# Kernel tuning notes

Hardware: AMD Instinct MI355X
Metric: run time of the kernel (lower is better)

The kernel has to match this reference:

```python
import jax, jax.numpy as jnp
import numpy as np
import math

N = 1500; E = 24000; C_IN = 16; H = 64; NUM_LAYERS = 10; RATIO = 0.9
NEG = -1e9


def setup_inputs() -> dict:
    key = jax.random.key(0)
    ks = jax.random.split(key, 40)
    it = iter(range(40))
    def nrm(shape, scale=0.1):
        return jax.random.normal(ks[next(it)], shape, dtype=jnp.float32) * scale
    src = jax.random.randint(ks[next(it)], (E,), 0, N, dtype=jnp.int32)
    off = jax.random.randint(ks[next(it)], (E,), 1, N, dtype=jnp.int32)
    dst = (src + off) % N  # no self loops in the raw edge list
    return dict(
        x=nrm((N, C_IN), 1.0),
        edge_src=src, edge_dst=dst,
        W1=nrm((C_IN, H // 2)), b1=jnp.zeros((H // 2,), jnp.float32),
        W2=nrm((H // 2, H)), b2=jnp.zeros((H,), jnp.float32),
        W3=nrm((H, H)), b3=jnp.zeros((H,), jnp.float32),
        Wrel=nrm((NUM_LAYERS - 1, H, H)), brel=jnp.zeros((NUM_LAYERS - 1, H), jnp.float32),
        Wroot=nrm((NUM_LAYERS - 1, H, H)),
        pW=nrm((4, H, H)), pb=jnp.zeros((4, H), jnp.float32),
        leW1=nrm((4, H, 1)), leb1=jnp.zeros((4, 1), jnp.float32),
        leW2=nrm((4, H, 1)),
        leW3=nrm((4, H, 1)), leb3=jnp.zeros((4, 1), jnp.float32),
        linW1=nrm((NUM_LAYERS * H, H)), linb1=jnp.zeros((H,), jnp.float32),
        linW2=nrm((H, 10)), linb2=jnp.zeros((10,), jnp.float32),
    )


def _seg_mean(vals, idx, n):
    s = jax.ops.segment_sum(vals, idx, num_segments=n)
    c = jax.ops.segment_sum(jnp.ones((idx.shape[0],), vals.dtype), idx, num_segments=n)
    return s / jnp.maximum(c, 1.0)[:, None]


def _feast(x, W, b, srcL, dstL, n):
    # FeaStConv with heads=1: softmax over a single head == 1 -> mean of lin(x_j) + bias
    return _seg_mean((x @ W)[srcL], dstL, n) + b


def _gconv_sparse(x, src, dst, Wr, br, Wo, n):
    return _seg_mean(x[src], dst, n) @ Wr + br + x @ Wo


def _gconv_dense(x, A, Wr, br, Wo):
    # mean aggregation: divide weighted sum by count of (nonzero) in-edges
    Mf = (A != 0).astype(x.dtype)
    agg = (A.T @ x) / jnp.maximum(Mf.sum(0), 1.0)[:, None]
    return agg @ Wr + br + x @ Wo


def _topk_pool(xc, fitness, ratio):
    k = int(math.ceil(ratio * xc.shape[0]))
    fit_k, perm = jax.lax.top_k(fitness, k)
    return xc[perm] * fit_k[:, None], perm


def _asap_sparse(x, src, dst, pW, pb, leW1, leb1, leW2, leW3, leb3):
    n = x.shape[0]
    ar = jnp.arange(n, dtype=src.dtype)
    srcL = jnp.concatenate([src, ar])  # add remaining self loops (weight 1)
    dstL = jnp.concatenate([dst, ar])
    xq = jax.ops.segment_max(x[srcL], dstL, num_segments=n) @ pW + pb
    s = jax.nn.leaky_relu(jnp.sum(xq[dstL] * x[srcL], -1), 0.2)
    m = jax.ops.segment_max(s, dstL, num_segments=n)
    e = jnp.exp(s - m[dstL])
    score = e / jax.ops.segment_sum(e, dstL, num_segments=n)[dstL]
    xc = jax.ops.segment_sum(x[srcL] * score[:, None], dstL, num_segments=n)
    # LEConv fitness score (edge weight = 1)
    a = xc @ leW1 + leb1
    b = xc @ leW2
    agg = jax.ops.segment_sum(a[srcL] - b[dstL], dstL, num_segments=n)
    fitness = jax.nn.sigmoid((agg + xc @ leW3 + leb3)[:, 0])
    x_new, perm = _topk_pool(xc, fitness, RATIO)
    S = jnp.zeros((n, n), x.dtype).at[srcL, dstL].add(score)
    A = jnp.zeros((n, n), x.dtype).at[srcL, dstL].add(1.0)
    Sp = S[:, perm]
    A_new = Sp.T @ A @ Sp
    k = A_new.shape[0]
    return x_new, A_new * (1.0 - jnp.eye(k, dtype=x.dtype))  # remove diag


def _asap_dense(x, A, pW, pb, leW1, leb1, leW2, leW3, leb3):
    n = x.shape[0]
    A = A + jnp.diag((jnp.diag(A) == 0).astype(A.dtype))  # add remaining self loops
    M = A != 0
    Mf = M.astype(x.dtype)
    xq = jnp.max(jnp.where(M[:, :, None], x[:, None, :], NEG), axis=0) @ pW + pb  # [n,H]
    Sc = jnp.where(M, jax.nn.leaky_relu(x @ xq.T, 0.2), NEG)  # [j,i]
    m = Sc.max(0)
    e = jnp.where(M, jnp.exp(Sc - m), 0.0)
    score = e / e.sum(0)
    xc = score.T @ x
    a = xc @ leW1 + leb1
    b = xc @ leW2
    agg = Mf.T @ a - Mf.sum(0)[:, None] * b
    fitness = jax.nn.sigmoid((agg + xc @ leW3 + leb3)[:, 0])
    x_new, perm = _topk_pool(xc, fitness, RATIO)
    Sp = score[:, perm]
    A_new = Sp.T @ A @ Sp
    k = A_new.shape[0]
    return x_new, A_new * (1.0 - jnp.eye(k, dtype=x.dtype))


def _forward(x, edge_src, edge_dst, W1, b1, W2, b2, W3, b3, Wrel, brel, Wroot,
             pW, pb, leW1, leb1, leW2, leW3, leb3, linW1, linb1, linW2, linb2):
    n = x.shape[0]
    ar = jnp.arange(n, dtype=edge_src.dtype)
    srcL = jnp.concatenate([edge_src, ar])  # FeaStConv add_self_loops=True
    dstL = jnp.concatenate([edge_dst, ar])
    x = jax.nn.elu(_feast(x, W1, b1, srcL, dstL, n))
    x = jax.nn.elu(_feast(x, W2, b2, srcL, dstL, n))
    x = jax.nn.elu(_feast(x, W3, b3, srcL, dstL, n))
    xs = [x.mean(0, keepdims=True)]  # single graph -> global_mean_pool == mean
    A = None
    for i in range(NUM_LAYERS - 1):
        if A is None:
            x = jax.nn.relu(_gconv_sparse(x, edge_src, edge_dst, Wrel[i], brel[i], Wroot[i], x.shape[0]))
        else:
            x = jax.nn.relu(_gconv_dense(x, A, Wrel[i], brel[i], Wroot[i]))
        xs.append(x.mean(0, keepdims=True))
        if i % 2 == 0 and i < NUM_LAYERS - 2:
            p = i // 2
            args = (pW[p], pb[p], leW1[p], leb1[p], leW2[p], leW3[p], leb3[p])
            if A is None:
                x, A = _asap_sparse(x, edge_src, edge_dst, *args)
            else:
                x, A = _asap_dense(x, A, *args)
    h = jnp.concatenate(xs, axis=-1)  # [1, NUM_LAYERS*H] jumping-knowledge cat
    h = jax.nn.relu(h @ linW1 + linb1)
    return jax.nn.log_softmax(h @ linW2 + linb2, axis=-1)


def reference(x, edge_src, edge_dst, W1, b1, W2, b2, W3, b3, Wrel, brel, Wroot,
              pW, pb, leW1, leb1, leW2, leW3, leb3, linW1, linb1, linW2, linb2):
    return _forward(x, edge_src, edge_dst, W1, b1, W2, b2, W3, b3, Wrel, brel, Wroot,
                    pW, pb, leW1, leb1, leW2, leW3, leb3, linW1, linb1, linW2, linb2)
```

## Files before the change

### kernel.cpp

```cpp
#include <hip/hip_runtime.h>
#include <math.h>

#define NEGV -1000000000.0f

typedef short short8 __attribute__((ext_vector_type(8)));
typedef float floatx4 __attribute__((ext_vector_type(4)));

__device__ __forceinline__ float sigm(float x){ return 1.0f/(1.0f+expf(-x)); }
__device__ __forceinline__ void edge_sd(int e,const int* src,const int* dst,int E,int& s,int& d){
  if(e<E){ s=src[e]; d=dst[e]; } else { s=e-E; d=s; }
}
__device__ __forceinline__ ushort bf16rn(float x){
  unsigned u = __float_as_uint(x);
  unsigned r = (u + 0x7fffu + ((u>>16)&1u)) >> 16;
  return (ushort)r;
}
__device__ __forceinline__ float bf16f(ushort h){ return __uint_as_float(((unsigned)h)<<16); }

__global__ void k_zero(float* __restrict__ p, size_t n){
  size_t i = (size_t)blockIdx.x*256 + threadIdx.x;
  if (i < n) p[i] = 0.0f;
}

__global__ void k_split3(const float* __restrict__ src,int R,int Cs,int ld,
                         ushort* __restrict__ dst,int Cp,int bmode){
  int idx = blockIdx.x*256+threadIdx.x;
  if (idx >= R*Cp) return;
  int r = idx / Cp, c = idx - r*Cp;
  float x = (c < Cs) ? src[(size_t)r*ld + c] : 0.0f;
  ushort h = bf16rn(x);
  ushort l = bf16rn(x - bf16f(h));
  size_t base = (size_t)r*(3*Cp) + c;
  dst[base]        = h;
  dst[base + Cp]   = bmode ? l : h;
  dst[base + 2*Cp] = bmode ? h : l;
}
__global__ void k_split3_Tdual(const float* __restrict__ src,int Rs,int Cs,int ld,
                               const int* __restrict__ gperm,const float* __restrict__ cscale,
                               const float* __restrict__ emax,
                               ushort* __restrict__ dstA,ushort* __restrict__ dstB,
                               ushort* __restrict__ dstCpad,int Kp){
  __shared__ float t[32][33];
  int tx = threadIdx.x & 31, ty = threadIdx.x >> 5;
  int kb = blockIdx.y*32, xb = blockIdx.x*32;
  int x = xb + tx;
  int gx = (x < Cs) ? gperm[x] : 0;
#pragma unroll
  for (int i=0;i<4;i++){
    int k = kb + ty + i*8;
    t[ty+i*8][tx] = (k < Rs && x < Cs) ? src[(size_t)k*ld + gx] : 0.0f;
  }
  __syncthreads();
  const int K3 = 3*Kp;
#pragma unroll
  for (int i=0;i<4;i++){
    int xo = xb + ty + i*8, ko = kb + tx;
    if (xo < Cs){
      float v = 0.0f;
      if (ko < Rs){
        int g = gperm[xo];
        v = expf(t[tx][ty+i*8] - emax[g]) * cscale[g];
      }
      ushort h = bf16rn(v);
      ushort l = bf16rn(v - bf16f(h));
      size_t base = (size_t)xo*K3 + ko;
      dstA[base] = h; dstA[base+Kp] = h; dstA[base+2*Kp] = l;
      dstB[base] = h; dstB[base+Kp] = l; dstB[base+2*Kp] = h;
      if (ko >= Rs){ dstCpad[base]=0; dstCpad[base+Kp]=0; dstCpad[base+2*Kp]=0; }
    }
  }
}

template<int EPI>
__global__ __launch_bounds__(256) void k_gemm_mfma(
    const ushort* __restrict__ A, const ushort* __restrict__ B,
    float* __restrict__ C, int ldc, int M, int N, int K3,
    const float* __restrict__ mask, int ldm)
{
  __shared__ ushort As[2][64][72];
  __shared__ ushort Bs[2][64][72];
  const int tid = threadIdx.x;
  const int m0 = blockIdx.y*64, n0 = blockIdx.x*64;
  const int w = tid>>6, lane = tid&63;
  const int lo4 = lane&15, quad = lane>>4;
  const int sr = tid>>2, sseg = tid&3;

  floatx4 acc[4];
#pragma unroll
  for(int c=0;c<4;c++){ acc[c][0]=0.f; acc[c][1]=0.f; acc[c][2]=0.f; acc[c][3]=0.f; }

  const size_t arow = (size_t)(m0+sr)*K3;
  const size_t brow = (size_t)(n0+sr)*K3;
  const bool aval = (m0+sr) < M;
  const bool bval = (n0+sr) < N;

  uint4 av0 = make_uint4(0,0,0,0), av1 = make_uint4(0,0,0,0);
  uint4 bv0 = make_uint4(0,0,0,0), bv1 = make_uint4(0,0,0,0);
  if (aval){ av0 = *(const uint4*)(A + arow + sseg*8);
             av1 = *(const uint4*)(A + arow + 32 + sseg*8); }
  if (bval){ bv0 = *(const uint4*)(B + brow + sseg*8);
             bv1 = *(const uint4*)(B + brow + 32 + sseg*8); }
  *(uint4*)&As[0][sr][sseg*8] = av0; *(uint4*)&As[0][sr][32+sseg*8] = av1;
  *(uint4*)&Bs[0][sr][sseg*8] = bv0; *(uint4*)&Bs[0][sr][32+sseg*8] = bv1;
  __syncthreads();

  const int T = K3 >> 6;
  for (int i=0;i<T;i++){
    const int cb = i & 1;
    if (i+1 < T){
      const int k0 = (i+1)<<6;
      av0 = make_uint4(0,0,0,0); av1 = make_uint4(0,0,0,0);
      bv0 = make_uint4(0,0,0,0); bv1 = make_uint4(0,0,0,0);
      if (aval){ av0 = *(const uint4*)(A + arow + k0 + sseg*8);
                 av1 = *(const uint4*)(A + arow + k0 + 32 + sseg*8); }
      if (bval){ bv0 = *(const uint4*)(B + brow + k0 + sseg*8);
                 bv1 = *(const uint4*)(B + brow + k0 + 32 + sseg*8); }
    }
    short8 af0 = *(const short8*)&As[cb][16*w + lo4][quad*8];
    short8 af1 = *(const short8*)&As[cb][16*w + lo4][32+quad*8];
#pragma unroll
    for (int c=0;c<4;c++){
      short8 bf0 = *(const short8*)&Bs[cb][16*c + lo4][quad*8];
      acc[c] = __builtin_amdgcn_mfma_f32_16x16x32_bf16(af0, bf0, acc[c], 0, 0, 0);
      short8 bf1 = *(const short8*)&Bs[cb][16*c + lo4][32+quad*8];
      acc[c] = __builtin_amdgcn_mfma_f32_16x16x32_bf16(af1, bf1, acc[c], 0, 0, 0);
    }
    if (i+1 < T){
      __syncthreads();
      *(uint4*)&As[1-cb][sr][sseg*8] = av0; *(uint4*)&As[1-cb][sr][32+sseg*8] = av1;
      *(uint4*)&Bs[1-cb][sr][sseg*8] = bv0; *(uint4*)&Bs[1-cb][sr][32+sseg*8] = bv1;
      __syncthreads();
    }
  }

#pragma unroll
  for (int c=0;c<4;c++){
    const int gn = n0 + 16*c + lo4;
#pragma unroll
    for (int r=0;r<4;r++){
      const int gm = m0 + 16*w + quad*4 + r;
      if (gm < M && gn < N){
        float v = acc[c][r];
        if (EPI==1) v = (mask[(size_t)gm*ldm+gn] != 0.0f || gm==gn) ? (v > 0.0f ? v : 0.2f*v) : NEGV;
        if (EPI==2 && gm==gn) v = 0.0f;
        C[(size_t)gm*ldc+gn] = v;
      }
    }
  }
}

__global__ __launch_bounds__(256) void k_gemm_mfma_tb(
    const ushort* __restrict__ A, const ushort* __restrict__ B,
    ushort* __restrict__ Cb, int Kp, int M, int N, int K3)
{
  __shared__ ushort As[2][64][72];
  __shared__ ushort Bs[2][64][72];
  const int tid = threadIdx.x;
  const int m0 = blockIdx.y*64, n0 = blockIdx.x*64;
  const int w = tid>>6, lane = tid&63;
  const int lo4 = lane&15, quad = lane>>4;
  const int sr = tid>>2, sseg = tid&3;

  floatx4 acc[4];
#pragma unroll
  for(int c=0;c<4;c++){ acc[c][0]=0.f; acc[c][1]=0.f; acc[c][2]=0.f; acc[c][3]=0.f; }

  const size_t arow = (size_t)(m0+sr)*K3;
  const size_t brow = (size_t)(n0+sr)*K3;
  const bool aval = (m0+sr) < M;
  const bool bval = (n0+sr) < N;

  uint4 av0 = make_uint4(0,0,0,0), av1 = make_uint4(0,0,0,0);
  uint4 bv0 = make_uint4(0,0,0,0), bv1 = make_uint4(0,0,0,0);
  if (aval){ av0 = *(const uint4*)(A + arow + sseg*8);
             av1 = *(const uint4*)(A + arow + 32 + sseg*8); }
  if (bval){ bv0 = *(const uint4*)(B + brow + sseg*8);
             bv1 = *(const uint4*)(B + brow + 32 + sseg*8); }
  *(uint4*)&As[0][sr][sseg*8] = av0; *(uint4*)&As[0][sr][32+sseg*8] = av1;
  *(uint4*)&Bs[0][sr][sseg*8] = bv0; *(uint4*)&Bs[0][sr][32+sseg*8] = bv1;
  __syncthreads();

  const int T = K3 >> 6;
  for (int i=0;i<T;i++){
    const int cb = i & 1;
    if (i+1 < T){
      const int k0 = (i+1)<<6;
      av0 = make_uint4(0,0,0,0); av1 = make_uint4(0,0,0,0);
      bv0 = make_uint4(0,0,0,0); bv1 = make_uint4(0,0,0,0);
      if (aval){ av0 = *(const uint4*)(A + arow + k0 + sseg*8);
                 av1 = *(const uint4*)(A + arow + k0 + 32 + sseg*8); }
      if (bval){ bv0 = *(const uint4*)(B + brow + k0 + sseg*8);
                 bv1 = *(const uint4*)(B + brow + k0 + 32 + sseg*8); }
    }
    short8 af0 = *(const short8*)&As[cb][16*w + lo4][quad*8];
    short8 af1 = *(const short8*)&As[cb][16*w + lo4][32+quad*8];
#pragma unroll
    for (int c=0;c<4;c++){
      short8 bf0 = *(const short8*)&Bs[cb][16*c + lo4][quad*8];
      acc[c] = __builtin_amdgcn_mfma_f32_16x16x32_bf16(af0, bf0, acc[c], 0, 0, 0);
      short8 bf1 = *(const short8*)&Bs[cb][16*c + lo4][32+quad*8];
      acc[c] = __builtin_amdgcn_mfma_f32_16x16x32_bf16(af1, bf1, acc[c], 0, 0, 0);
    }
    if (i+1 < T){
      __syncthreads();
      *(uint4*)&As[1-cb][sr][sseg*8] = av0; *(uint4*)&As[1-cb][sr][32+sseg*8] = av1;
      *(uint4*)&Bs[1-cb][sr][sseg*8] = bv0; *(uint4*)&Bs[1-cb][sr][32+sseg*8] = bv1;
      __syncthreads();
    }
  }

  const int K3o = 3*Kp;
#pragma unroll
  for (int c=0;c<4;c++){
    const int gn = n0 + 16*c + lo4;
    if (gn < N){
#pragma unroll
      for (int r=0;r<4;r++){
        const int gm = m0 + 16*w + quad*4 + r;
        if (gm < M){
          size_t base = (size_t)gn*K3o + gm;
          float sp = bf16f(B[base]) + bf16f(B[base+Kp]);
          float v = acc[c][r] + sp;
          ushort h = bf16rn(v);
          ushort l = bf16rn(v - bf16f(h));
          Cb[base] = h; Cb[base+Kp] = l; Cb[base+2*Kp] = h;
        }
      }
    }
  }
}

template<bool MAXM, bool COUNT, bool EXPM, bool SELF>
__global__ __launch_bounds__(256) void k_skinny(
    const float* __restrict__ A, int lda,
    const float* __restrict__ X,
    const float* __restrict__ mcol,
    float* __restrict__ P, int* __restrict__ cntp,
    int M, int K, int kchunk)
{
  __shared__ float As[16][68];
  __shared__ float Xs[16][68];
  const int tid = threadIdx.x;
  const int m0 = blockIdx.y * 64;
  const int tmb = (tid & 15) * 4, tnb = (tid >> 4) * 4;
  float acc[4][4];
  int cacc[4] = {0,0,0,0};
#pragma unroll
  for (int i=0;i<4;i++)
#pragma unroll
    for (int j=0;j<4;j++) acc[i][j] = MAXM ? NEGV : 0.0f;

  const int kstart = blockIdx.z * kchunk;
  int kend = kstart + kchunk; if (kend > K) kend = K;
  const int ml = tid & 63, tb = tid >> 6;
  const bool mvalid = (m0 + ml) < M;
  float mc = 0.0f;
  if (EXPM && mvalid) mc = mcol[m0 + ml];

  for (int k0 = kstart; k0 < kend; k0 += 16) {
#pragma unroll
    for (int s=0;s<4;s++) {
      const int tk = tb + s*4;
      float va = 0.0f, vx = 0.0f;
      if ((k0+tk) < K) {
        if (mvalid){
          va = A[(size_t)(k0+tk)*lda + m0 + ml];
          if (EXPM) va = expf(va - mc);
        }
        vx = X[(size_t)(k0+tk)*64 + ml];
      }
      As[tk][ml] = va;
      Xs[tk][ml] = vx;
    }
    __syncthreads();
#pragma unroll
    for (int kk=0; kk<16; kk++) {
      const float4 a4 = *(const float4*)&As[kk][tmb];
      const float4 b4 = *(const float4*)&Xs[kk][tnb];
      const float av[4] = {a4.x,a4.y,a4.z,a4.w};
      const float bv[4] = {b4.x,b4.y,b4.z,b4.w};
#pragma unroll
      for (int i=0;i<4;i++){
        if (COUNT) cacc[i] += (av[i] != 0.0f) ? 1 : 0;
#pragma unroll
        for (int j=0;j<4;j++) {
          if (MAXM) acc[i][j] = fmaxf(acc[i][j], av[i] != 0.0f ? bv[j] : NEGV);
          else      acc[i][j] = fmaf(av[i], bv[j], acc[i][j]);
        }
      }
    }
    __syncthreads();
  }

  const size_t slab = (size_t)blockIdx.z * M * 64;
#pragma unroll
  for (int i=0;i<4;i++){
    const int m = m0 + tmb + i;
    if (m < M){
#pragma unroll
      for (int j=0;j<4;j++){
        float v = acc[i][j];
        if (SELF) v = fmaxf(v, X[(size_t)m*64 + tnb + j]);
        P[slab + (size_t)m*64 + tnb + j] = v;
      }
    }
  }
  if (COUNT && tnb == 0){
#pragma unroll
    for (int i=0;i<4;i++){
      const int m = m0 + tmb + i;
      if (m < M) cntp[blockIdx.z*M + m] = cacc[i];
    }
  }
}

__global__ __launch_bounds__(256) void k_poolq(
    const float* __restrict__ SEGP,const int* __restrict__ cntp8,int Z,
    const float* __restrict__ pWp,const float* __restrict__ pbp,
    const float* __restrict__ X,
    ushort* __restrict__ dstA,ushort* __restrict__ dstB,
    float* __restrict__ cntP,int n)
{
  __shared__ float xq[4][65];
  const int tid = threadIdx.x;
  const int r = tid>>6, j = tid&63;
  const int i = blockIdx.x*4 + r;
  float v = NEGV;
  if (i < n){
    for(int z=0;z<Z;z++) v = fmaxf(v, SEGP[(size_t)z*n*64 + (size_t)i*64 + j]);
    if (j == 0){
      int c=1; for(int z=0;z<Z;z++) c += cntp8[z*n+i];
      cntP[i] = (float)c;
    }
  }
  xq[r][j] = v;
  __syncthreads();
  if (i < n){
    float s = pbp[j];
    for(int q=0;q<64;q++) s = fmaf(xq[r][q], pWp[q*64+j], s);
    size_t base = (size_t)i*192 + j;
    ushort h = bf16rn(s), l = bf16rn(s - bf16f(h));
    dstB[base] = h; dstB[base+64] = l; dstB[base+128] = h;
    float x = X[(size_t)i*64 + j];
    h = bf16rn(x); l = bf16rn(x - bf16f(h));
    dstA[base] = h; dstA[base+64] = h; dstA[base+128] = l;
  }
}

__global__ __launch_bounds__(256) void k_gconv_fuse(
    const float* __restrict__ SEGP,const int* __restrict__ cntp8,int Z,
    const float* __restrict__ Wrel,const float* __restrict__ brel,
    const float* __restrict__ X,const float* __restrict__ Wroot,
    float* __restrict__ XN,int n,float* __restrict__ meanacc,float inv_n)
{
  __shared__ float agg_s[4][65];
  __shared__ float xrow[4][65];
  __shared__ float cnt_s[4];
  const int tid = threadIdx.x;
  const int r = tid>>6, j = tid&63;
  const int i = blockIdx.x*4 + r;
  float a = 0.0f;
  if (i < n){
    for(int z=0;z<Z;z++) a += SEGP[(size_t)z*n*64 + (size_t)i*64 + j];
    xrow[r][j] = X[(size_t)i*64 + j];
    if (j == 0){
      int c=0; for(int z=0;z<Z;z++) c += cntp8[z*n+i];
      cnt_s[r] = (float)(c>1?c:1);
    }
  }
  agg_s[r][j] = a;
  __syncthreads();
  float v = 0.0f;
  if (i < n){
    float acc=0.0f, rt=0.0f;
    for(int q=0;q<64;q++){
      acc = fmaf(agg_s[r][q], Wrel[q*64+j], acc);
      rt  = fmaf(xrow[r][q],  Wroot[q*64+j], rt);
    }
    v = fmaxf(acc/cnt_s[r] + brel[j] + rt, 0.0f);
    XN[(size_t)i*64 + j] = v;
  }
  __syncthreads();
  agg_s[r][j] = v;
  __syncthreads();
  if (r == 0) atomicAdd(&meanacc[j], (agg_s[0][j]+agg_s[1][j]+agg_s[2][j]+agg_s[3][j])*inv_n);
}

__global__ __launch_bounds__(256) void k_smax_fused(const float* __restrict__ S,int n,
                                                    float* __restrict__ mcol,float* __restrict__ invd){
  __shared__ float red[16][17];
  const int jc = threadIdx.x & 15, rg = threadIdx.x >> 4;
  const int j = blockIdx.x*16 + jc;
  float m = -3.0e38f;
  if (j < n)
    for(int i=rg;i<n;i+=16) m = fmaxf(m, S[(size_t)i*n+j]);
  red[rg][jc] = m;
  __syncthreads();
  for(int s=8;s>0;s>>=1){
    if(rg<s) red[rg][jc] = fmaxf(red[rg][jc], red[rg+s][jc]);
    __syncthreads();
  }
  const float mc = red[0][jc];
  __syncthreads();
  float sum = 0.0f;
  if (j < n)
    for(int i=rg;i<n;i+=16) sum += expf(S[(size_t)i*n+j]-mc);
  red[rg][jc] = sum;
  __syncthreads();
  for(int s=8;s>0;s>>=1){
    if(rg<s) red[rg][jc] += red[rg+s][jc];
    __syncthreads();
  }
  if(rg==0 && j<n){ mcol[j]=mc; invd[j]=1.0f/red[0][jc]; }
}

__global__ __launch_bounds__(256) void k_xcabc_dense(
    const float* __restrict__ SEGP,int Z,const float* __restrict__ invd,
    float* __restrict__ XC,
    const float* __restrict__ w1,const float* bb1,const float* __restrict__ w2,
    const float* __restrict__ w3,const float* bb3,
    float* aN,float* bN,float* cN,int* pcnt,int n)
{
  __shared__ float xc[4][65];
  const int tid = threadIdx.x;
  const int r = tid>>6, j = tid&63;
  const int i = blockIdx.x*4 + r;
  if (blockIdx.x==0 && tid==0) *pcnt = 0;
  float v = 0.0f;
  if (i < n){
    for(int z=0;z<Z;z++) v += SEGP[(size_t)z*n*64 + (size_t)i*64 + j];
    v *= invd[i];
    XC[(size_t)i*64+j] = v;
  }
  xc[r][j] = v;
  __syncthreads();
  if (i < n && j < 3){
    float s = (j==0)?bb1[0]:((j==2)?bb3[0]:0.0f);
    const float* w = (j==0)?w1:((j==1)?w2:w3);
    for(int q=0;q<64;q++) s = fmaf(xc[r][q], w[q], s);
    if(j==0) aN[i]=s; else if(j==1) bN[i]=s; else cN[i]=s;
  }
}

__global__ void k_aggcol(const float* __restrict__ A,const float* __restrict__ aN,
                         float* __restrict__ aggp,int n){
  int idx = blockIdx.x*256+threadIdx.x; if(idx>=n*16) return;
  int j = idx % n, c = idx / n;
  int i0 = (int)(((long long)n*c)/16), i1 = (int)(((long long)n*(c+1))/16);
  float s = 0.0f;
  for(int i=i0;i<i1;i++) if(A[(size_t)i*n + j] != 0.0f) s += aN[i];
  aggp[c*n + j] = s;
}

template<int MODE>
__global__ __launch_bounds__(256) void k_rank_fused(
    const float* __restrict__ fit_in,
    const float* __restrict__ aggp,const float* __restrict__ cntP,
    const float* __restrict__ aN,const float* __restrict__ bN,const float* __restrict__ cN,
    const float* __restrict__ XC,float* __restrict__ XN,
    int n,int k,int* pcnt,int* perm)
{
  __shared__ float fs[1504];
  const int tid = threadIdx.x;
  for(int u=tid; u<n; u+=256){
    float f;
    if (MODE==0) f = fit_in[u];
    else {
      float a = aN[u];
      for(int c=0;c<16;c++) a += aggp[c*n+u];
      f = sigm(a - cntP[u]*bN[u] + cN[u]);
    }
    fs[u] = f;
  }
  __syncthreads();
  const int v = blockIdx.x*256+tid; if(v>=n) return;
  const float fv = fs[v]; int r = 0;
  for(int u=0;u<n;u++){ float fu = fs[u]; r += (fu > fv || (fu == fv && u < v)) ? 1 : 0; }
  if (r < k){
    int p = atomicAdd(pcnt,1);
    perm[p] = v;
    const float* src = XC + (size_t)v*64;
    float* d = XN + (size_t)p*64;
    for(int h=0;h<64;h++) d[h] = src[h]*fv;
  }
}

__global__ void k_deg(const int* __restrict__ src,const int* __restrict__ dst,int* indeg,int* outdeg,int E){
  int e = blockIdx.x*256+threadIdx.x; if(e>=E) return;
  atomicAdd(&indeg[dst[e]],1); atomicAdd(&outdeg[src[e]],1);
}
__global__ __launch_bounds__(256) void k_prefix2(const int* __restrict__ indeg,const int* __restrict__ outdeg,
                          int* offD,int* curD,int* offS,int* curS,int n){
  __shared__ int ds[1504];
  const int* dsrc = blockIdx.y ? outdeg : indeg;
  for(int u=threadIdx.x; u<n; u+=256) ds[u] = dsrc[u];
  __syncthreads();
  int t = blockIdx.x*256+threadIdx.x; if(t>n) return;
  int s = 0;
  for(int u=0;u<t;u++) s += ds[u]+1;
  if (blockIdx.y){ offS[t]=s; if(t<n) curS[t]=s; }
  else           { offD[t]=s; if(t<n) curD[t]=s; }
}
__global__ void k_csr_fill2(const int* src,const int* dst,
                            int* curS,int* colS,int* eidS,
                            int* curD,int* rowD,int* eidD,int E,int n){
  int e = blockIdx.x*256+threadIdx.x; if(e>=E+n) return;
  int s,d; edge_sd(e,src,dst,E,s,d);
  int p = atomicAdd(&curS[s],1); colS[p]=d; eidS[p]=e;
  int q = atomicAdd(&curD[d],1); rowD[q]=s; eidD[q]=e;
}

__global__ void k_mm_small(const float* __restrict__ A,const float* __restrict__ W,
                           const float* __restrict__ b,float* __restrict__ C,
                           int M,int K,int Np,int act){
  int idx = blockIdx.x*256+threadIdx.x; if(idx>=M*Np) return;
  int m = idx/Np, j = idx - m*Np;
  float s = b ? b[j] : 0.0f;
  const float* a = A + (size_t)m*K;
  for(int q=0;q<K;q++) s = fmaf(a[q], W[(size_t)q*Np + j], s);
  if(act==1) s = fmaxf(s, 0.0f);
  C[idx] = s;
}

__global__ void k_feast_gf(const float* __restrict__ Y,const int* __restrict__ offD,
                           const int* __restrict__ rowD,
                           const float* __restrict__ b,float* X,int n,int H,
                           float* __restrict__ meanacc,float inv_n){
  __shared__ float ms[4][64];
  int idx = blockIdx.x*256+threadIdx.x;
  float v = 0.0f;
  if(idx<n*H){
    int i = idx/H, h = idx - i*H;
    int p0 = offD[i], p1 = offD[i+1];
    float s = 0.0f;
    for(int p=p0;p<p1;p++) s += Y[(size_t)rowD[p]*H + h];
    float t = s/(float)(p1-p0) + b[h];
    v = t > 0.0f ? t : (expf(t)-1.0f);
    X[idx] = v;
  }
  if(meanacc){
    int r = threadIdx.x>>6, j = threadIdx.x&63;
    ms[r][j] = (idx<n*H) ? v : 0.0f;
    __syncthreads();
    if(r==0) atomicAdd(&meanacc[j], (ms[0][j]+ms[1][j]+ms[2][j]+ms[3][j])*inv_n);
  }
}

__global__ __launch_bounds__(256) void k_gconv_sparse_f(
    const float* __restrict__ X,const int* __restrict__ offD,const int* __restrict__ rowD,
    const int* __restrict__ eidD,int E,
    const float* __restrict__ Wrel,const float* __restrict__ brel,
    const float* __restrict__ Wroot,
    float* __restrict__ XN,int n,float* __restrict__ meanacc,float inv_n)
{
  __shared__ float agg_s[4][65];
  __shared__ float xrow[4][65];
  __shared__ float cnt_s[4];
  const int tid = threadIdx.x;
  const int r = tid>>6, j = tid&63;
  const int i = blockIdx.x*4 + r;
  float a = 0.0f;
  if (i < n){
    int p0 = offD[i], p1 = offD[i+1], c = 0;
    for(int p=p0;p<p1;p++){
      if (eidD[p] < E){ a += X[(size_t)rowD[p]*64 + j]; c++; }
    }
    xrow[r][j] = X[(size_t)i*64 + j];
    if (j == 0) cnt_s[r] = (float)(c>1?c:1);
  }
  agg_s[r][j] = a;
  __syncthreads();
  float v = 0.0f;
  if (i < n){
    float acc=0.0f, rt=0.0f;
    for(int q=0;q<64;q++){
      acc = fmaf(agg_s[r][q], Wrel[q*64+j], acc);
      rt  = fmaf(xrow[r][q],  Wroot[q*64+j], rt);
    }
    v = fmaxf(acc/cnt_s[r] + brel[j] + rt, 0.0f);
    XN[(size_t)i*64 + j] = v;
  }
  __syncthreads();
  agg_s[r][j] = v;
  __syncthreads();
  if (r == 0) atomicAdd(&meanacc[j], (agg_s[0][j]+agg_s[1][j]+agg_s[2][j]+agg_s[3][j])*inv_n);
}

__global__ __launch_bounds__(256) void k_xqmaxq(
    const float* __restrict__ X,const int* __restrict__ offD,const int* __restrict__ rowD,
    const float* __restrict__ pWp,const float* __restrict__ pbp,
    float* __restrict__ XQ2,int n)
{
  __shared__ float xq[4][65];
  const int tid = threadIdx.x;
  const int r = tid>>6, j = tid&63;
  const int i = blockIdx.x*4 + r;
  float v = -3.0e38f;
  if (i < n){
    int p0 = offD[i], p1 = offD[i+1];
    for(int p=p0;p<p1;p++) v = fmaxf(v, X[(size_t)rowD[p]*64 + j]);
  }
  xq[r][j] = v;
  __syncthreads();
  if (i < n){
    float s = pbp[j];
    for(int q=0;q<64;q++) s = fmaf(xq[r][q], pWp[q*64+j], s);
    XQ2[(size_t)i*64+j] = s;
  }
}

__global__ void k_edge_score(const int* __restrict__ src,const int* __restrict__ dst,
                             const float* __restrict__ XQ2,const float* __restrict__ X,
                             float* sE,int E,int n){
  int e = blockIdx.x*256+threadIdx.x; if(e>=E+n) return;
  int s,d; edge_sd(e,src,dst,E,s,d);
  const float* q = XQ2 + (size_t)d*64;
  const float* x = X + (size_t)s*64;
  float acc = 0.0f;
  for(int h=0;h<64;h++) acc = fmaf(q[h], x[h], acc);
  sE[e] = acc > 0.0f ? acc : 0.2f*acc;
}

__global__ void k_dstsoft(const int* __restrict__ offD,const int* __restrict__ eidD,
                          const float* __restrict__ sE,float* __restrict__ scE,int n){
  int i = blockIdx.x*256+threadIdx.x; if(i>=n) return;
  int p0 = offD[i], p1 = offD[i+1];
  float m = -3.0e38f;
  for(int p=p0;p<p1;p++) m = fmaxf(m, sE[eidD[p]]);
  float d = 0.0f;
  for(int p=p0;p<p1;p++) d += expf(sE[eidD[p]]-m);
  float inv = 1.0f/d;
  for(int p=p0;p<p1;p++){ int e = eidD[p]; scE[e] = expf(sE[e]-m)*inv; }
}

__global__ __launch_bounds__(256) void k_xcabc0(
    const int* __restrict__ offD,const int* __restrict__ rowD,const int* __restrict__ eidD,
    const float* __restrict__ scE,const float* __restrict__ X,
    float* __restrict__ XC,
    const float* __restrict__ w1,const float* bb1,const float* __restrict__ w2,
    const float* __restrict__ w3,const float* bb3,
    float* aN,float* bN,float* cN,int* pcnt,int n)
{
  __shared__ float xc[4][65];
  const int tid = threadIdx.x;
  const int r = tid>>6, j = tid&63;
  const int i = blockIdx.x*4 + r;
  if (blockIdx.x==0 && tid==0) *pcnt = 0;
  float v = 0.0f;
  if (i < n){
    int p0 = offD[i], p1 = offD[i+1];
    for(int p=p0;p<p1;p++) v += scE[eidD[p]] * X[(size_t)rowD[p]*64 + j];
    XC[(size_t)i*64+j] = v;
  }
  xc[r][j] = v;
  __syncthreads();
  if (i < n && j < 3){
    float s = (j==0)?bb1[0]:((j==2)?bb3[0]:0.0f);
    const float* w = (j==0)?w1:((j==1)?w2:w3);
    for(int q=0;q<64;q++) s = fmaf(xc[r][q], w[q], s);
    if(j==0) aN[i]=s; else if(j==1) bN[i]=s; else cN[i]=s;
  }
}

__global__ void k_aggfit0(const int* __restrict__ offD,const int* __restrict__ rowD,
                          const float* aN,const float* bN,const float* cN,
                          float* fit,int n){
  int i = blockIdx.x*256+threadIdx.x; if(i>=n) return;
  int p0 = offD[i], p1 = offD[i+1];
  float s = 0.0f;
  for(int p=p0;p<p1;p++) s += aN[rowD[p]];
  fit[i] = sigm(s - (float)(p1-p0)*bN[i] + cN[i]);
}

__global__ void k_stage1n(const int* src,const int* dst,const int* __restrict__ offS,
                          const int* __restrict__ colS,const int* __restrict__ eidS,
                          const float* __restrict__ scE,
                          float* R,int E,int n){
  int e = blockIdx.x*256+threadIdx.x; if(e>=E+n) return;
  int i,j; edge_sd(e,src,dst,E,i,j);
  int p0 = offS[j], p1 = offS[j+1];
  float* Ri = R + (size_t)i*n;
  for(int p=p0;p<p1;p++) atomicAdd(&Ri[colS[p]], scE[eidS[p]]);
}
__global__ void k_stage2p(const int* __restrict__ perm,const int* __restrict__ offD,
                          const int* __restrict__ rowD,const int* __restrict__ eidD,
                          const float* __restrict__ scE,
                          const float* __restrict__ R,float* A,int k,int n){
  int idx = blockIdx.x*256+threadIdx.x; if(idx>=k*k) return;
  int u = idx/k, v = idx - u*k;
  int d = perm[u], pv = perm[v];
  float acc = 0.0f;
  int p0 = offD[d], p1 = offD[d+1];
  for(int p=p0;p<p1;p++) acc = fmaf(scE[eidD[p]], R[(size_t)rowD[p]*n + pv], acc);
  A[idx] = (u==v) ? 0.0f : acc;
}

__global__ void k_head2(const float* __restrict__ xs,const float* __restrict__ W1,
                        const float* __restrict__ b1,const float* __restrict__ W2,
                        const float* __restrict__ b2,float* out){
  __shared__ float h2[64];
  __shared__ float lg[10];
  int t = threadIdx.x;
  float s = b1[t];
  for(int q=0;q<640;q++) s = fmaf(xs[q], W1[q*64+t], s);
  h2[t] = fmaxf(s, 0.0f);
  __syncthreads();
  if(t < 10){
    float s2 = b2[t];
    for(int k=0;k<64;k++) s2 = fmaf(h2[k], W2[k*10+t], s2);
    lg[t] = s2;
  }
  __syncthreads();
  if(t == 0){
    float mx = lg[0];
    for(int i=1;i<10;i++) mx = fmaxf(mx, lg[i]);
    float se = 0.0f;
    for(int i=0;i<10;i++) se += expf(lg[i]-mx);
    float lse = mx + logf(se);
    for(int i=0;i<10;i++) out[i] = lg[i]-lse;
  }
}

extern "C" void kernel_launch(void* const* d_in, const int* in_sizes, int n_in,
                              void* d_out, int out_size, void* d_ws, size_t ws_size,
                              hipStream_t stream) {
  const int N0 = 1500, E = 24000, Z = 16, L = E + N0;
  const float* x0   = (const float*)d_in[0];
  const int* esrc   = (const int*)d_in[1];
  const int* edst   = (const int*)d_in[2];
  const float* W1   = (const float*)d_in[3];  const float* b1   = (const float*)d_in[4];
  const float* W2   = (const float*)d_in[5];  const float* b2   = (const float*)d_in[6];
  const float* W3   = (const float*)d_in[7];  const float* b3   = (const float*)d_in[8];
  const float* Wrel = (const float*)d_in[9];  const float* brel = (const float*)d_in[10];
  const float* Wroot= (const float*)d_in[11];
  const float* pW   = (const float*)d_in[12]; const float* pb   = (const float*)d_in[13];
  const float* leW1 = (const float*)d_in[14]; const float* leb1 = (const float*)d_in[15];
  const float* leW2 = (const float*)d_in[16]; const float* leW3 = (const float*)d_in[17];
  const float* leb3 = (const float*)d_in[18];
  const float* linW1= (const float*)d_in[19]; const float* linb1= (const float*)d_in[20];
  const float* linW2= (const float*)d_in[21]; const float* linb2= (const float*)d_in[22];
  float* out = (float*)d_out;

  float* ws = (float*)d_ws;
  size_t cur = 0;
  auto allocF = [&](size_t nf)->float*{ float* p = ws + cur; cur += (nf + 15) & ~(size_t)15; return p; };
  float* xs   = allocF(640);
  int* indeg  = (int*)allocF(1504);
  int* outdeg = (int*)allocF(1504);
  float* Xa  = allocF(96000); float* Xb  = allocF(96000); float* Y   = allocF(96000);
  float* XQ2 = allocF(96000); float* XC  = allocF(96000);
  float* mcol = allocF(1504); float* invd = allocF(1504);
  float* aN = allocF(1504); float* bN = allocF(1504); float* cN = allocF(1504);
  float* fit = allocF(1504); float* cntP = allocF(1504);
  int* pcnt = (int*)allocF(16);
  int* perm = (int*)allocF(1504);
  int* offD = (int*)allocF(1504); int* offS = (int*)allocF(1504);
  int* curD = (int*)allocF(1504); int* curS = (int*)allocF(1504);
  int* colS = (int*)allocF(25504); int* eidS = (int*)allocF(25504);
  int* rowD = (int*)allocF(25504); int* eidD = (int*)allocF(25504);
  float* sE = allocF(25504); float* scE = allocF(25504);
  int* cntp8 = (int*)allocF((size_t)Z*1504);
  float* aggp = allocF(16*1504);
  float* SEGP = allocF((size_t)Z*1504*64);
  float* Rbig = allocF((size_t)1500*1500);
  float* SCb  = Rbig;
  float* A0  = allocF((size_t)1350*1350);
  float* A1s = allocF((size_t)1350*1350);
  const size_t BFSZ = (size_t)1350*4224/2 + 32;
  ushort* Abf = (ushort*)allocF(BFSZ);
  ushort* Bbf = (ushort*)allocF(BFSZ);
  ushort* Cbf = (ushort*)allocF(BFSZ);
  ushort* Dbf = (ushort*)allocF(BFSZ);

  dim3 B256(256);
  auto G1 = [&](size_t n){ return dim3((unsigned)((n + 255) / 256)); };
  auto ZF = [&](void* p, size_t nfloats){ k_zero<<<G1(nfloats),B256,0,stream>>>((float*)p, nfloats); };
  auto kcz = [&](int K){ return (int)(((K + Z*16 - 1) / (Z*16)) * 16); };

  ZF(xs, 640 + 1504 + 1504);
  k_deg<<<G1(E),B256,0,stream>>>(esrc, edst, indeg, outdeg, E);
  k_prefix2<<<dim3((N0+256)/256,2),B256,0,stream>>>(indeg, outdeg, offD, curD, offS, curS, N0);
  k_csr_fill2<<<G1(L),B256,0,stream>>>(esrc, edst, curS, colS, eidS, curD, rowD, eidD, E, N0);

  auto feast = [&](const float* xin,int cin,const float* W,const float* bb,int hh,float* xout,float* macc){
    k_mm_small<<<G1((size_t)N0*hh),B256,0,stream>>>(xin, W, nullptr, Y, N0, cin, hh, 0);
    k_feast_gf<<<G1((size_t)N0*hh),B256,0,stream>>>(Y, offD, rowD, bb, xout, N0, hh, macc, 1.0f/N0);
  };
  feast(x0, 16, W1, b1, 32, Xa, nullptr);
  feast(Xa, 32, W2, b2, 64, Xb, nullptr);
  feast(Xb, 64, W3, b3, 64, Xa, xs + 0);
  float* X = Xa; float* XN = Xb;

  k_gconv_sparse_f<<<dim3((N0+3)/4),B256,0,stream>>>(X, offD, rowD, eidD, E, Wrel, brel, Wroot,
                                                     XN, N0, xs + 64, 1.0f/N0);
  { float* t = X; X = XN; XN = t; }

  {
    const int n = 1500, kk = 1350;
    k_xqmaxq<<<dim3((n+3)/4),B256,0,stream>>>(X, offD, rowD, pW, pb, XQ2, n);
    k_edge_score<<<G1(L),B256,0,stream>>>(esrc, edst, XQ2, X, sE, E, n);
    k_dstsoft<<<G1(n),B256,0,stream>>>(offD, eidD, sE, scE, n);
    k_xcabc0<<<dim3((n+3)/4),B256,0,stream>>>(offD, rowD, eidD, scE, X, XC,
                                              leW1, leb1, leW2, leW3, leb3, aN, bN, cN, pcnt, n);
    k_aggfit0<<<G1(n),B256,0,stream>>>(offD, rowD, aN, bN, cN, fit, n);
    k_rank_fused<0><<<G1(n),B256,0,stream>>>(fit, nullptr, nullptr, nullptr, nullptr, nullptr,
                                             XC, XN, n, kk, pcnt, perm);
    ZF(Rbig, (size_t)n*n);
    k_stage1n<<<G1(L),B256,0,stream>>>(esrc, edst, offS, colS, eidS, scE, Rbig, E, n);
    k_stage2p<<<G1((size_t)kk*kk),B256,0,stream>>>(perm, offD, rowD, eidD, scE, Rbig, A0, kk, n);
    { float* t = X; X = XN; XN = t; }
  }

  float* Acur = A0; float* Aoth = A1s;
  int nn = 1350;

  auto gconv_dense = [&](int layer){
    dim3 g(1, (nn+63)/64, Z);
    k_skinny<false,true,false,false><<<g,B256,0,stream>>>(Acur, nn, X, nullptr, SEGP, cntp8, nn, nn, kcz(nn));
    k_gconv_fuse<<<dim3((nn+3)/4),B256,0,stream>>>(SEGP, cntp8, Z,
        Wrel + (size_t)layer*4096, brel + layer*64, X, Wroot + (size_t)layer*4096,
        XN, nn, xs + (size_t)(layer+1)*64, 1.0f/nn);
    { float* t = X; X = XN; XN = t; }
  };

  auto asap_dense = [&](int kk, int p){
    {
      dim3 g(1, (nn+63)/64, Z);
      k_skinny<true,true,false,true><<<g,B256,0,stream>>>(Acur, nn, X, nullptr, SEGP, cntp8, nn, nn, kcz(nn));
    }
    k_poolq<<<dim3((nn+3)/4),B256,0,stream>>>(SEGP, cntp8, Z, pW + (size_t)p*4096, pb + p*64,
                                              X, Abf, Bbf, cntP, nn);
    {
      dim3 g((nn+63)/64, (nn+63)/64);
      k_gemm_mfma<1><<<g,B256,0,stream>>>(Abf, Bbf, SCb, nn, nn, nn, 192, Acur, nn);
    }
    k_smax_fused<<<dim3((nn+15)/16),B256,0,stream>>>(SCb, nn, mcol, invd);
    {
      dim3 g(1, (nn+63)/64, Z);
      k_skinny<false,false,true,false><<<g,B256,0,stream>>>(SCb, nn, X, mcol, SEGP, nullptr, nn, nn, kcz(nn));
    }
    k_xcabc_dense<<<dim3((nn+3)/4),B256,0,stream>>>(SEGP, Z, invd, XC,
        leW1 + p*64, leb1 + p, leW2 + p*64, leW3 + p*64, leb3 + p, aN, bN, cN, pcnt, nn);
    k_aggcol<<<G1((size_t)nn*16),B256,0,stream>>>(Acur, aN, aggp, nn);
    k_rank_fused<1><<<G1(nn),B256,0,stream>>>(nullptr, aggp, cntP, aN, bN, cN,
                                              XC, XN, nn, kk, pcnt, perm);
    const int Kp = (nn + 63) & ~63;
    const int K3 = 3*Kp;
    k_split3<<<G1((size_t)nn*Kp),B256,0,stream>>>(Acur, nn, nn, nn, Abf, Kp, 0);
    { dim3 gt((kk+31)/32, Kp/32);
      k_split3_Tdual<<<gt,B256,0,stream>>>(SCb, nn, kk, nn, perm, invd, mcol, Dbf, Bbf, Cbf, Kp); }
    { dim3 g((kk+63)/64, (nn+63)/64);
      k_gemm_mfma_tb<<<g,B256,0,stream>>>(Abf, Bbf, Cbf, Kp, nn, kk, K3); }
    { dim3 g((kk+63)/64, (kk+63)/64);
      k_gemm_mfma<2><<<g,B256,0,stream>>>(Dbf, Cbf, Aoth, kk, kk, kk, K3, nullptr, 0); }
    { float* t = X; X = XN; XN = t; }
    { float* t = Acur; Acur = Aoth; Aoth = t; }
    nn = kk;
  };

  gconv_dense(1);
  gconv_dense(2);
  asap_dense(1215, 1);
  gconv_dense(3);
  gconv_dense(4);
  asap_dense(1094, 2);
  gconv_dense(5);
  gconv_dense(6);
  asap_dense(985, 3);
  gconv_dense(7);
  gconv_dense(8);

  k_head2<<<1,64,0,stream>>>(xs, linW1, linb1, linW2, linb2, out);
}
```

Measured before the change: 1.509 ms.

## Split-K the pooled adjacency GEMMs into two partials plus reduction kernels

The two MFMA GEMMs in dense ASAP pooling (A·S and Sᵀ·(AS)) now run as split-K over two z-slices that write fp32 partials. Separate reduction kernels sum the partials, apply the bf16 split epilogue (transposed through shared memory) and zero the diagonal. This roughly doubles the block count for these small ~1000² GEMMs to fill more CUs. It costs extra launches and partial-buffer traffic, and reuses scratch buffers (Rbig, Aoth, SEGP) for the partials. The shared-memory load row mapping is also permuted.

```diff
diff --git a/kernel.cpp b/kernel.cpp
--- a/kernel.cpp
+++ b/kernel.cpp
@@ -142,16 +142,16 @@
       if (gm < M && gn < N){
         float v = acc[c][r];
         if (EPI==1) v = (mask[(size_t)gm*ldm+gn] != 0.0f || gm==gn) ? (v > 0.0f ? v : 0.2f*v) : NEGV;
-        if (EPI==2 && gm==gn) v = 0.0f;
         C[(size_t)gm*ldc+gn] = v;
       }
     }
   }
 }
 
-__global__ __launch_bounds__(256) void k_gemm_mfma_tb(
+__global__ __launch_bounds__(256) void k_gemm_pp(
     const ushort* __restrict__ A, const ushort* __restrict__ B,
-    ushort* __restrict__ Cb, int Kp, int M, int N, int K3)
+    float* __restrict__ P0, float* __restrict__ P1, int ldp,
+    int M, int N, int K3, int kchunk)
 {
   __shared__ ushort As[2][64][72];
   __shared__ ushort Bs[2][64][72];
@@ -159,14 +159,23 @@
   const int m0 = blockIdx.y*64, n0 = blockIdx.x*64;
   const int w = tid>>6, lane = tid&63;
   const int lo4 = lane&15, quad = lane>>4;
-  const int sr = tid>>2, sseg = tid&3;
+  const int l6 = tid & 63;
+  const int rw = (((l6>>2)&3)<<1) | ((l6>>4)&1) | (((l6>>5)&1)<<3);
+  const int sr = ((tid>>6)<<4) | rw;
+  const int sseg = tid&3;
+
+  const int z = blockIdx.z;
+  float* __restrict__ P = z ? P1 : P0;
+  const int kbeg = z * kchunk;
+  int klen = K3 - kbeg; if (klen > kchunk) klen = kchunk;
+  const int T = klen >> 6;
 
   floatx4 acc[4];
 #pragma unroll
   for(int c=0;c<4;c++){ acc[c][0]=0.f; acc[c][1]=0.f; acc[c][2]=0.f; acc[c][3]=0.f; }
 
-  const size_t arow = (size_t)(m0+sr)*K3;
-  const size_t brow = (size_t)(n0+sr)*K3;
+  const size_t arow = (size_t)(m0+sr)*K3 + kbeg;
+  const size_t brow = (size_t)(n0+sr)*K3 + kbeg;
   const bool aval = (m0+sr) < M;
   const bool bval = (n0+sr) < N;
 
@@ -180,7 +189,6 @@
   *(uint4*)&Bs[0][sr][sseg*8] = bv0; *(uint4*)&Bs[0][sr][32+sseg*8] = bv1;
   __syncthreads();
 
-  const int T = K3 >> 6;
   for (int i=0;i<T;i++){
     const int cb = i & 1;
     if (i+1 < T){
@@ -209,25 +217,54 @@
     }
   }
 
-  const int K3o = 3*Kp;
 #pragma unroll
   for (int c=0;c<4;c++){
     const int gn = n0 + 16*c + lo4;
-    if (gn < N){
-#pragma unroll
-      for (int r=0;r<4;r++){
-        const int gm = m0 + 16*w + quad*4 + r;
-        if (gm < M){
-          size_t base = (size_t)gn*K3o + gm;
-          float sp = bf16f(B[base]) + bf16f(B[base+Kp]);
-          float v = acc[c][r] + sp;
-          ushort h = bf16rn(v);
-          ushort l = bf16rn(v - bf16f(h));
-          Cb[base] = h; Cb[base+Kp] = l; Cb[base+2*Kp] = h;
-        }
-      }
-    }
-  }
+#pragma unroll
+    for (int r=0;r<4;r++){
+      const int gm = m0 + 16*w + quad*4 + r;
+      if (gm < M && gn < N) P[(size_t)gm*ldp+gn] = acc[c][r];
+    }
+  }
+}
+
+__global__ __launch_bounds__(256) void k_red_tb(
+    const float* __restrict__ P0,const float* __restrict__ P1,int ldp,
+    const ushort* __restrict__ Bb, ushort* __restrict__ Cb,
+    int M,int N,int Kp)
+{
+  __shared__ float t[32][33];
+  const int tx = threadIdx.x & 31, ty = threadIdx.x >> 5;
+  const int mb = blockIdx.y*32, nb = blockIdx.x*32;
+  const int n = nb + tx;
+#pragma unroll
+  for (int i=0;i<4;i++){
+    int m = mb + ty + i*8;
+    float v = 0.0f;
+    if (m < M && n < N){ size_t o = (size_t)m*ldp + n; v = P0[o] + P1[o]; }
+    t[ty+i*8][tx] = v;
+  }
+  __syncthreads();
+  const int K3o = 3*Kp;
+#pragma unroll
+  for (int i=0;i<4;i++){
+    int no = nb + ty + i*8, mo = mb + tx;
+    if (no < N && mo < M){
+      size_t base = (size_t)no*K3o + mo;
+      float sp = bf16f(Bb[base]) + bf16f(Bb[base+Kp]);
+      float v = t[tx][ty+i*8] + sp;
+      ushort h = bf16rn(v), l = bf16rn(v - bf16f(h));
+      Cb[base] = h; Cb[base+Kp] = l; Cb[base+2*Kp] = h;
+    }
+  }
+}
+
+__global__ void k_red_diag(const float* __restrict__ P0,const float* __restrict__ P1,
+                           float* __restrict__ C,int kk){
+  int idx = blockIdx.x*256+threadIdx.x;
+  if (idx >= kk*kk) return;
+  int u = idx/kk, v = idx - u*kk;
+  C[idx] = (u==v) ? 0.0f : (P0[idx] + P1[idx]);
 }
 
 template<bool MAXM, bool COUNT, bool EXPM, bool SELF>
@@ -849,10 +886,23 @@
     k_split3<<<G1((size_t)nn*Kp),B256,0,stream>>>(Acur, nn, nn, nn, Abf, Kp, 0);
     { dim3 gt((kk+31)/32, Kp/32);
       k_split3_Tdual<<<gt,B256,0,stream>>>(SCb, nn, kk, nn, perm, invd, mcol, Dbf, Bbf, Cbf, Kp); }
-    { dim3 g((kk+63)/64, (nn+63)/64);
-      k_gemm_mfma_tb<<<g,B256,0,stream>>>(Abf, Bbf, Cbf, Kp, nn, kk, K3); }
-    { dim3 g((kk+63)/64, (kk+63)/64);
-      k_gemm_mfma<2><<<g,B256,0,stream>>>(Dbf, Cbf, Aoth, kk, kk, kk, K3, nullptr, 0); }
+    const int Tk = K3 >> 6;
+    const int kchunk = ((Tk + 1) >> 1) << 6;
+    {
+      float* PT0 = Rbig;
+      float* PT1 = Aoth;
+      dim3 g((kk+63)/64, (nn+63)/64, 2);
+      k_gemm_pp<<<g,B256,0,stream>>>(Abf, Bbf, PT0, PT1, kk, nn, kk, K3, kchunk);
+      dim3 gr((kk+31)/32, (nn+31)/32);
+      k_red_tb<<<gr,B256,0,stream>>>(PT0, PT1, kk, Bbf, Cbf, nn, kk, Kp);
+    }
+    {
+      float* PD0 = Rbig;
+      float* PD1 = SEGP;
+      dim3 g((kk+63)/64, (kk+63)/64, 2);
+      k_gemm_pp<<<g,B256,0,stream>>>(Dbf, Cbf, PD0, PD1, kk, kk, kk, K3, kchunk);
+      k_red_diag<<<G1((size_t)kk*kk),B256,0,stream>>>(PD0, PD1, Aoth, kk);
+    }
     { float* t = X; X = XN; XN = t; }
     { float* t = Acur; Acur = Aoth; Aoth = t; }
     nn = kk;
```

Measured after the change: 1.450 ms. 1.04x faster.
